# Kernel optimization log

Hardware: AMD Instinct MI355X
Metric: run time of the kernel (lower is better)

## Reference

```python
import jax, jax.numpy as jnp
import numpy as np

B, T, E, D = 64, 128, 4, 128
K = 4 * D  # ffn_hidden_dim
AUX_COEF = 0.01


def setup_inputs() -> dict:
    key = jax.random.key(0)
    ks = jax.random.split(key, 7)
    return {
        "x": jax.random.normal(ks[0], (B, T, D), dtype=jnp.float32),
        "expert_w1": jax.random.normal(ks[1], (T, E, D, K), dtype=jnp.float32) * 0.02,
        "expert_b1": jnp.zeros((T, E, K), dtype=jnp.float32),
        "expert_w2": jax.random.normal(ks[2], (T, E, K, D), dtype=jnp.float32) * 0.02,
        "expert_b2": jnp.zeros((T, E, D), dtype=jnp.float32),
        # router_train nn.Linear(D, E): store as [D, E] plus bias [E]
        "router_w": jax.random.normal(ks[3], (D, E), dtype=jnp.float32) * (1.0 / np.sqrt(D)),
        "router_b": jax.random.normal(ks[4], (E,), dtype=jnp.float32) * 0.01,
    }


def reference(x, expert_w1, expert_b1, expert_w2, expert_b2, router_w, router_b):
    # training=True path with use_relu_routing=True
    router_logits = jnp.einsum("btd,de->bte", x, router_w) + router_b  # [B,T,E]
    gates = jax.nn.relu(router_logits)
    gates = gates / (gates.sum(axis=-1, keepdims=True) + 1e-9)

    # per-token, per-expert 2-layer FFN
    hidden = jnp.einsum("btd,tedk->btek", x, expert_w1) + expert_b1  # [B,T,E,K]
    hidden = jax.nn.gelu(hidden, approximate=False)  # torch F.gelu default = exact erf
    expert_outputs = jnp.einsum("btek,tekd->bted", hidden, expert_w2) + expert_b2  # [B,T,E,D]

    output = (expert_outputs * gates[..., None]).sum(axis=2)  # [B,T,D]
    aux_loss = AUX_COEF * gates.sum() / (x.shape[0] * x.shape[1])
    return output, aux_loss
```

## Files before the change

### kernel.cpp

```cpp
#include <hip/hip_runtime.h>
#include <hip/hip_bf16.h>

#define NB 64
#define NT 128
#define NE 4
#define ND 128
#define NK 512

typedef __attribute__((ext_vector_type(8))) short bf16x8;
typedef __attribute__((ext_vector_type(4))) float f32x4;

__device__ __forceinline__ short f2bf(float f) {
    union { __hip_bfloat16 b; short s; } u;
    u.b = __float2bfloat16(f);
    return u.s;
}

__device__ __forceinline__ bf16x8 cvt8(const float* f) {
    bf16x8 r;
    #pragma unroll
    for (int j = 0; j < 8; ++j) r[j] = f2bf(f[j]);
    return r;
}

__device__ __forceinline__ float gelu_erf(float x) {
    return 0.5f * x * (1.0f + erff(x * 0.70710678118654752f));
}

__global__ __launch_bounds__(256)
void moe_gates(const float* __restrict__ x,
               const float* __restrict__ rw,
               const float* __restrict__ rb,
               float* __restrict__ gates_ws,
               float* __restrict__ aux_partial)
{
    const int tid  = threadIdx.x;
    const int lane = tid & 63;
    const int wave = tid >> 6;
    __shared__ float waux[4];

    const float4 rw0 = *(const float4*)(rw + lane * 4);
    const float4 rw1 = *(const float4*)(rw + (64 + lane) * 4);
    const float4 rbv = *(const float4*)rb;

    float aux = 0.f;
    #pragma unroll
    for (int i = 0; i < 4; ++i) {
        const int tok = (blockIdx.x * 4 + wave) * 4 + i;
        const float x0 = x[tok * ND + lane];
        const float x1 = x[tok * ND + 64 + lane];
        float p0 = x0 * rw0.x + x1 * rw1.x;
        float p1 = x0 * rw0.y + x1 * rw1.y;
        float p2 = x0 * rw0.z + x1 * rw1.z;
        float p3 = x0 * rw0.w + x1 * rw1.w;
        #pragma unroll
        for (int off = 32; off > 0; off >>= 1) {
            p0 += __shfl_xor(p0, off);
            p1 += __shfl_xor(p1, off);
            p2 += __shfl_xor(p2, off);
            p3 += __shfl_xor(p3, off);
        }
        if (lane == 0) {
            p0 = fmaxf(p0 + rbv.x, 0.f);
            p1 = fmaxf(p1 + rbv.y, 0.f);
            p2 = fmaxf(p2 + rbv.z, 0.f);
            p3 = fmaxf(p3 + rbv.w, 0.f);
            const float s   = p0 + p1 + p2 + p3;
            const float inv = 1.f / (s + 1e-9f);
            float4 g; g.x = p0 * inv; g.y = p1 * inv; g.z = p2 * inv; g.w = p3 * inv;
            *(float4*)(gates_ws + tok * NE) = g;
            aux += s * inv;
        }
    }
    if (lane == 0) waux[wave] = aux;
    __syncthreads();
    if (tid == 0)
        aux_partial[blockIdx.x] = waux[0] + waux[1] + waux[2] + waux[3];
}

__global__ __launch_bounds__(256, 2)
void moe_main(const float* __restrict__ x,
              const float* __restrict__ w1,
              const float* __restrict__ b1,
              const float* __restrict__ w2,
              const float* __restrict__ b2,
              const float* __restrict__ gates_ws,
              float* __restrict__ ws)
{
    const int bid  = blockIdx.x;
    const int t    = bid >> 2;
    const int e    = bid & 3;
    const int tid  = threadIdx.x;
    const int lane = tid & 63;
    const int wave = tid >> 6;
    const int l15  = lane & 15;
    const int l4   = lane >> 4;

    __shared__ short Hs[NB][NK + 8];
    __shared__ float gate_s[NB];

    if (tid < NB)
        gate_s[tid] = gates_ws[(tid * NT + t) * NE + e];

    const float* W1 = w1 + (size_t)((t * NE + e) * ND) * NK;
    const float* B1 = b1 + (t * NE + e) * NK;
    const int n0 = wave * 128;

    f32x4 acc[4][8];
    #pragma unroll
    for (int m = 0; m < 4; ++m)
        #pragma unroll
        for (int n = 0; n < 8; ++n) acc[m][n] = (f32x4){0.f, 0.f, 0.f, 0.f};

    {
        const float* wbase = W1 + (size_t)(l4 * 8) * NK + n0 + l15;
        float wbuf[4][8];
        #pragma unroll
        for (int q = 0; q < 4; ++q) {
            const float* wp = wbase + q * 16;
            #pragma unroll
            for (int j = 0; j < 8; ++j) wbuf[q][j] = wp[(size_t)j * NK];
        }

        bf16x8 afr[4];
        #pragma unroll
        for (int p = 0; p < 32; ++p) {
            const int ks = p >> 3, nt = p & 7;
            if (nt == 0) {
                const int d0 = ks * 32 + l4 * 8;
                #pragma unroll
                for (int m = 0; m < 4; ++m) {
                    const float* xp = x + (size_t)((m * 16 + l15) * NT + t) * ND + d0;
                    float xf[8];
                    *(float4*)&xf[0] = *(const float4*)(xp);
                    *(float4*)&xf[4] = *(const float4*)(xp + 4);
                    afr[m] = cvt8(xf);
                }
            }
            const bf16x8 bfr = cvt8(wbuf[p & 3]);
            if (p < 28) {
                const int p4 = p + 4;
                const int ks4 = p4 >> 3, nt4 = p4 & 7;
                const float* wp = wbase + (size_t)(ks4 * 32) * NK + nt4 * 16;
                #pragma unroll
                for (int j = 0; j < 8; ++j) wbuf[p4 & 3][j] = wp[(size_t)j * NK];
            }
            #pragma unroll
            for (int m = 0; m < 4; ++m)
                acc[m][nt] = __builtin_amdgcn_mfma_f32_16x16x32_bf16(afr[m], bfr, acc[m][nt], 0, 0, 0);
        }
    }

    #pragma unroll
    for (int nt = 0; nt < 8; ++nt) {
        const int n = n0 + nt * 16 + l15;
        const float bb = B1[n];
        #pragma unroll
        for (int m = 0; m < 4; ++m) {
            const int row = m * 16 + l4 * 4;
            #pragma unroll
            for (int r = 0; r < 4; ++r) {
                const float hh = acc[m][nt][r] + bb;
                Hs[row + r][n] = f2bf(gelu_erf(hh));
            }
        }
    }
    __syncthreads();

    const float* W2 = w2 + (size_t)((t * NE + e) * NK) * ND;
    const float* B2 = b2 + (t * NE + e) * ND;
    const int c0 = wave * 32;

    f32x4 acc2[4][2];
    #pragma unroll
    for (int m = 0; m < 4; ++m)
        #pragma unroll
        for (int n = 0; n < 2; ++n) acc2[m][n] = (f32x4){0.f, 0.f, 0.f, 0.f};

    {
        const float* w2base = W2 + (size_t)(l4 * 8) * ND + c0 + l15;
        float wb2[4][8];
        #pragma unroll
        for (int q = 0; q < 4; ++q) {
            const int ksq = q >> 1, ntq = q & 1;
            const float* wp = w2base + (size_t)(ksq * 32) * ND + ntq * 16;
            #pragma unroll
            for (int j = 0; j < 8; ++j) wb2[q][j] = wp[(size_t)j * ND];
        }

        bf16x8 a2[4];
        #pragma unroll
        for (int p = 0; p < 32; ++p) {
            const int ks = p >> 1, nt = p & 1;
            if (nt == 0) {
                const int k0 = ks * 32 + l4 * 8;
                #pragma unroll
                for (int m = 0; m < 4; ++m)
                    a2[m] = *(const bf16x8*)(&Hs[m * 16 + l15][k0]);
            }
            const bf16x8 bfr = cvt8(wb2[p & 3]);
            if (p < 28) {
                const int p4 = p + 4;
                const int ks4 = p4 >> 1, nt4 = p4 & 1;
                const float* wp = w2base + (size_t)(ks4 * 32) * ND + nt4 * 16;
                #pragma unroll
                for (int j = 0; j < 8; ++j) wb2[p4 & 3][j] = wp[(size_t)j * ND];
            }
            #pragma unroll
            for (int m = 0; m < 4; ++m)
                acc2[m][nt] = __builtin_amdgcn_mfma_f32_16x16x32_bf16(a2[m], bfr, acc2[m][nt], 0, 0, 0);
        }
    }

    #pragma unroll
    for (int nt = 0; nt < 2; ++nt) {
        const int c = c0 + nt * 16 + l15;
        const float bb = B2[c];
        #pragma unroll
        for (int m = 0; m < 4; ++m) {
            #pragma unroll
            for (int r = 0; r < 4; ++r) {
                const int b = m * 16 + l4 * 4 + r;
                const float v = (acc2[m][nt][r] + bb) * gate_s[b];
                ws[(size_t)(e * NB * NT + b * NT + t) * ND + c] = v;
            }
        }
    }
}

__global__ __launch_bounds__(256)
void moe_reduce(const float* __restrict__ ws,
                const float* __restrict__ aux_partial,
                float* __restrict__ out)
{
    const int i = blockIdx.x * blockDim.x + threadIdx.x;
    const int stride = NB * NT * ND / 4;
    const float4* w = (const float4*)ws;
    const float4 a = w[i];
    const float4 b = w[i + stride];
    const float4 c = w[i + 2 * stride];
    const float4 d = w[i + 3 * stride];
    float4 r;
    r.x = a.x + b.x + c.x + d.x;
    r.y = a.y + b.y + c.y + d.y;
    r.z = a.z + b.z + c.z + d.z;
    r.w = a.w + b.w + c.w + d.w;
    ((float4*)out)[i] = r;

    if (blockIdx.x == 0) {
        const int tid = threadIdx.x;
        float s = aux_partial[tid] + aux_partial[tid + 256];
        #pragma unroll
        for (int off = 32; off > 0; off >>= 1) s += __shfl_xor(s, off);
        __shared__ float wsum[4];
        if ((tid & 63) == 0) wsum[tid >> 6] = s;
        __syncthreads();
        if (tid == 0)
            out[NB * NT * ND] = (wsum[0] + wsum[1] + wsum[2] + wsum[3]) *
                                (0.01f / (NB * NT));
    }
}

__global__ __launch_bounds__(256, 2)
void moe_main_fb(const float* __restrict__ x,
                 const float* __restrict__ w1,
                 const float* __restrict__ b1,
                 const float* __restrict__ w2,
                 const float* __restrict__ b2,
                 const float* __restrict__ rw,
                 const float* __restrict__ rb,
                 float* __restrict__ out)
{
    const int blk  = blockIdx.x;
    const int t    = blk >> 2;
    const int e    = blk & 3;
    const int tid  = threadIdx.x;
    const int lane = tid & 63;
    const int wave = tid >> 6;
    const int l15  = lane & 15;
    const int l4   = lane >> 4;

    __shared__ short Hs[NB][NK + 8];
    __shared__ float gate_s[NB];

    if (tid < NB) {
        const int b = tid;
        const float* xr = x + (b * NT + t) * ND;
        float l0 = rb[0], l1 = rb[1], l2 = rb[2], l3 = rb[3];
        #pragma unroll 8
        for (int d = 0; d < ND; ++d) {
            const float xv = xr[d];
            const float* w = rw + d * NE;
            l0 += xv * w[0]; l1 += xv * w[1]; l2 += xv * w[2]; l3 += xv * w[3];
        }
        l0 = fmaxf(l0, 0.f); l1 = fmaxf(l1, 0.f); l2 = fmaxf(l2, 0.f); l3 = fmaxf(l3, 0.f);
        const float ss  = l0 + l1 + l2 + l3;
        const float inv = 1.f / (ss + 1e-9f);
        const float ge  = (e == 0) ? l0 : (e == 1) ? l1 : (e == 2) ? l2 : l3;
        gate_s[b] = ge * inv;
        if (e == 0) {
            float aux = ss * inv;
            #pragma unroll
            for (int off = 32; off > 0; off >>= 1) aux += __shfl_down(aux, off);
            if (lane == 0) atomicAdd(out + NB * NT * ND, aux * (0.01f / (NB * NT)));
        }
    }
    __syncthreads();

    const float* W1 = w1 + (size_t)((t * NE + e) * ND) * NK;
    const float* B1 = b1 + (t * NE + e) * NK;
    const int n0 = wave * 128;

    f32x4 acc[4][8];
    #pragma unroll
    for (int m = 0; m < 4; ++m)
        #pragma unroll
        for (int n = 0; n < 8; ++n) acc[m][n] = (f32x4){0.f, 0.f, 0.f, 0.f};

    #pragma unroll
    for (int ks = 0; ks < 4; ++ks) {
        const int d0 = ks * 32 + l4 * 8;
        bf16x8 afr[4];
        #pragma unroll
        for (int m = 0; m < 4; ++m) {
            const int b = m * 16 + l15;
            const float* xp = x + (b * NT + t) * ND + d0;
            float xf[8];
            *(float4*)&xf[0] = *(const float4*)(xp);
            *(float4*)&xf[4] = *(const float4*)(xp + 4);
            afr[m] = cvt8(xf);
        }
        #pragma unroll
        for (int nt = 0; nt < 8; ++nt) {
            const int n = n0 + nt * 16 + l15;
            const float* wp = W1 + (size_t)d0 * NK + n;
            float wf[8];
            #pragma unroll
            for (int j = 0; j < 8; ++j) wf[j] = wp[(size_t)j * NK];
            const bf16x8 bfr = cvt8(wf);
            #pragma unroll
            for (int m = 0; m < 4; ++m)
                acc[m][nt] = __builtin_amdgcn_mfma_f32_16x16x32_bf16(afr[m], bfr, acc[m][nt], 0, 0, 0);
        }
    }

    #pragma unroll
    for (int nt = 0; nt < 8; ++nt) {
        const int n = n0 + nt * 16 + l15;
        const float bb = B1[n];
        #pragma unroll
        for (int m = 0; m < 4; ++m) {
            const int row = m * 16 + l4 * 4;
            #pragma unroll
            for (int r = 0; r < 4; ++r) {
                const float hh = acc[m][nt][r] + bb;
                Hs[row + r][n] = f2bf(gelu_erf(hh));
            }
        }
    }
    __syncthreads();

    const float* W2 = w2 + (size_t)((t * NE + e) * NK) * ND;
    const float* B2 = b2 + (t * NE + e) * ND;
    const int c0 = wave * 32;

    f32x4 acc2[4][2];
    #pragma unroll
    for (int m = 0; m < 4; ++m)
        #pragma unroll
        for (int n = 0; n < 2; ++n) acc2[m][n] = (f32x4){0.f, 0.f, 0.f, 0.f};

    #pragma unroll 4
    for (int ks = 0; ks < 16; ++ks) {
        const int k0 = ks * 32 + l4 * 8;
        bf16x8 afr[4];
        #pragma unroll
        for (int m = 0; m < 4; ++m)
            afr[m] = *(const bf16x8*)(&Hs[m * 16 + l15][k0]);
        #pragma unroll
        for (int nt = 0; nt < 2; ++nt) {
            const int c = c0 + nt * 16 + l15;
            const float* wp = W2 + (size_t)k0 * ND + c;
            float wf[8];
            #pragma unroll
            for (int j = 0; j < 8; ++j) wf[j] = wp[(size_t)j * ND];
            const bf16x8 bfr = cvt8(wf);
            #pragma unroll
            for (int m = 0; m < 4; ++m)
                acc2[m][nt] = __builtin_amdgcn_mfma_f32_16x16x32_bf16(afr[m], bfr, acc2[m][nt], 0, 0, 0);
        }
    }

    #pragma unroll
    for (int nt = 0; nt < 2; ++nt) {
        const int c = c0 + nt * 16 + l15;
        const float bb = B2[c];
        #pragma unroll
        for (int m = 0; m < 4; ++m) {
            #pragma unroll
            for (int r = 0; r < 4; ++r) {
                const int b = m * 16 + l4 * 4 + r;
                const float v = (acc2[m][nt][r] + bb) * gate_s[b];
                atomicAdd(out + (size_t)(b * NT + t) * ND + c, v);
            }
        }
    }
}

extern "C" void kernel_launch(void* const* d_in, const int* in_sizes, int n_in,
                              void* d_out, int out_size, void* d_ws, size_t ws_size,
                              hipStream_t stream) {
    const float* x  = (const float*)d_in[0];
    const float* w1 = (const float*)d_in[1];
    const float* b1 = (const float*)d_in[2];
    const float* w2 = (const float*)d_in[3];
    const float* b2 = (const float*)d_in[4];
    const float* rw = (const float*)d_in[5];
    const float* rb = (const float*)d_in[6];
    float* out = (float*)d_out;

    const size_t contrib_elems = (size_t)NE * NB * NT * ND;
    const size_t gates_elems   = (size_t)NB * NT * NE;
    const size_t aux_elems     = 512;
    const size_t ws_need = (contrib_elems + gates_elems + aux_elems) * sizeof(float);

    if (ws_size >= ws_need) {
        float* contrib = (float*)d_ws;
        float* gates   = contrib + contrib_elems;
        float* auxp    = gates + gates_elems;

        moe_gates<<<512, 256, 0, stream>>>(x, rw, rb, gates, auxp);
        moe_main<<<NT * NE, 256, 0, stream>>>(x, w1, b1, w2, b2, gates, contrib);
        moe_reduce<<<(NB * NT * ND / 4) / 256, 256, 0, stream>>>(contrib, auxp, out);
    } else {
        hipMemsetAsync(d_out, 0, (size_t)(NB * NT * ND + 1) * sizeof(float), stream);
        moe_main_fb<<<NT * NE, 256, 0, stream>>>(x, w1, b1, w2, b2, rw, rb, out);
    }
}
```

Before: 70.71 us.

## Stage expert weights through LDS with coalesced float4 loads and double buffering

Weights used to be loaded straight from global memory with a column-strided scalar gather per lane. They are now read with coalesced float4 loads, converted to bf16 and staged in shared memory. W1 is double-buffered across 4 k-stages, and W2 is prefetched several stages ahead in registers before being written to an LDS buffer. This is meant to improve global memory coalescing and bandwidth. In exchange it uses about 75KB of LDS (W1 buffers aliased with the H buffer), which may limit occupancy to one block per CU. It also adds extra barriers, and reading B fragments as strided 2-byte LDS loads may cause bank conflicts.

```diff
diff --git a/kernel.cpp b/kernel.cpp
--- a/kernel.cpp
+++ b/kernel.cpp
@@ -8,6 +8,7 @@
 #define NK 512
 
 typedef __attribute__((ext_vector_type(8))) short bf16x8;
+typedef __attribute__((ext_vector_type(4))) short bf16x4;
 typedef __attribute__((ext_vector_type(4))) float f32x4;
 
 __device__ __forceinline__ short f2bf(float f) {
@@ -20,6 +21,12 @@
     bf16x8 r;
     #pragma unroll
     for (int j = 0; j < 8; ++j) r[j] = f2bf(f[j]);
+    return r;
+}
+
+__device__ __forceinline__ bf16x4 cvt4(float4 f) {
+    bf16x4 r;
+    r[0] = f2bf(f.x); r[1] = f2bf(f.y); r[2] = f2bf(f.z); r[3] = f2bf(f.w);
     return r;
 }
 
@@ -96,15 +103,21 @@
     const int l15  = lane & 15;
     const int l4   = lane >> 4;
 
-    __shared__ short Hs[NB][NK + 8];
-    __shared__ float gate_s[NB];
+    __shared__ __align__(16) char smem[75008];
+    short* W1s    = (short*)smem;
+    short* Hs     = (short*)smem;
+    short* W2s    = (short*)(smem + 66560);
+    float* gate_s = (float*)(smem + 74752);
 
     if (tid < NB)
         gate_s[tid] = gates_ws[(tid * NT + t) * NE + e];
 
     const float* W1 = w1 + (size_t)((t * NE + e) * ND) * NK;
     const float* B1 = b1 + (t * NE + e) * NK;
+    const float* W2 = w2 + (size_t)((t * NE + e) * NK) * ND;
+    const float* B2 = b2 + (t * NE + e) * ND;
     const int n0 = wave * 128;
+    const int c0 = wave * 32;
 
     f32x4 acc[4][8];
     #pragma unroll
@@ -113,42 +126,78 @@
         for (int n = 0; n < 8; ++n) acc[m][n] = (f32x4){0.f, 0.f, 0.f, 0.f};
 
     {
-        const float* wbase = W1 + (size_t)(l4 * 8) * NK + n0 + l15;
-        float wbuf[4][8];
-        #pragma unroll
-        for (int q = 0; q < 4; ++q) {
-            const float* wp = wbase + q * 16;
-            #pragma unroll
-            for (int j = 0; j < 8; ++j) wbuf[q][j] = wp[(size_t)j * NK];
-        }
-
+        float4 wv[16];
+        #pragma unroll
+        for (int q = 0; q < 16; ++q) {
+            const int f = q * 256 + tid;
+            wv[q] = *(const float4*)(W1 + (size_t)(f >> 7) * NK + (f & 127) * 4);
+        }
+        #pragma unroll
+        for (int q = 0; q < 16; ++q) {
+            const int f = q * 256 + tid;
+            *(bf16x4*)&W1s[(f >> 7) * 512 + (f & 127) * 4] = cvt4(wv[q]);
+        }
+        __syncthreads();
+    }
+
+    #pragma unroll
+    for (int s = 0; s < 4; ++s) {
+        const int cur = s & 1;
+        float4 wv[16];
+        if (s < 3) {
+            #pragma unroll
+            for (int q = 0; q < 16; ++q) {
+                const int f = q * 256 + tid;
+                wv[q] = *(const float4*)(W1 + (size_t)((s + 1) * 32 + (f >> 7)) * NK + (f & 127) * 4);
+            }
+        }
         bf16x8 afr[4];
         #pragma unroll
-        for (int p = 0; p < 32; ++p) {
-            const int ks = p >> 3, nt = p & 7;
-            if (nt == 0) {
-                const int d0 = ks * 32 + l4 * 8;
-                #pragma unroll
-                for (int m = 0; m < 4; ++m) {
-                    const float* xp = x + (size_t)((m * 16 + l15) * NT + t) * ND + d0;
-                    float xf[8];
-                    *(float4*)&xf[0] = *(const float4*)(xp);
-                    *(float4*)&xf[4] = *(const float4*)(xp + 4);
-                    afr[m] = cvt8(xf);
-                }
-            }
-            const bf16x8 bfr = cvt8(wbuf[p & 3]);
-            if (p < 28) {
-                const int p4 = p + 4;
-                const int ks4 = p4 >> 3, nt4 = p4 & 7;
-                const float* wp = wbase + (size_t)(ks4 * 32) * NK + nt4 * 16;
-                #pragma unroll
-                for (int j = 0; j < 8; ++j) wbuf[p4 & 3][j] = wp[(size_t)j * NK];
-            }
+        for (int m = 0; m < 4; ++m) {
+            const float* xp = x + (size_t)((m * 16 + l15) * NT + t) * ND + s * 32 + l4 * 8;
+            float xf[8];
+            *(float4*)&xf[0] = *(const float4*)(xp);
+            *(float4*)&xf[4] = *(const float4*)(xp + 4);
+            afr[m] = cvt8(xf);
+        }
+        #pragma unroll
+        for (int nt = 0; nt < 8; ++nt) {
+            const int n = n0 + nt * 16 + l15;
+            bf16x8 bfr;
+            #pragma unroll
+            for (int j = 0; j < 8; ++j)
+                bfr[j] = W1s[cur * 16384 + (l4 * 8 + j) * 512 + n];
             #pragma unroll
             for (int m = 0; m < 4; ++m)
                 acc[m][nt] = __builtin_amdgcn_mfma_f32_16x16x32_bf16(afr[m], bfr, acc[m][nt], 0, 0, 0);
         }
+        if (s < 3) {
+            const int nxt = cur ^ 1;
+            #pragma unroll
+            for (int q = 0; q < 16; ++q) {
+                const int f = q * 256 + tid;
+                *(bf16x4*)&W1s[nxt * 16384 + (f >> 7) * 512 + (f & 127) * 4] = cvt4(wv[q]);
+            }
+        }
+        __syncthreads();
+    }
+
+    float4 w20[4];
+    float4 nv[3][4];
+    #pragma unroll
+    for (int q = 0; q < 4; ++q) {
+        const int f = q * 256 + tid;
+        w20[q] = *(const float4*)(W2 + (size_t)(f >> 5) * ND + (f & 31) * 4);
+    }
+    #pragma unroll
+    for (int q = 0; q < 4; ++q) {
+        const int f = q * 256 + tid;
+        nv[0][q] = *(const float4*)(W2 + (size_t)(32 + (f >> 5)) * ND + (f & 31) * 4);
+    }
+    #pragma unroll
+    for (int q = 0; q < 4; ++q) {
+        const int f = q * 256 + tid;
+        nv[1][q] = *(const float4*)(W2 + (size_t)(64 + (f >> 5)) * ND + (f & 31) * 4);
     }
 
     #pragma unroll
@@ -161,54 +210,56 @@
             #pragma unroll
             for (int r = 0; r < 4; ++r) {
                 const float hh = acc[m][nt][r] + bb;
-                Hs[row + r][n] = f2bf(gelu_erf(hh));
-            }
-        }
+                Hs[(row + r) * 520 + n] = f2bf(gelu_erf(hh));
+            }
+        }
+    }
+    #pragma unroll
+    for (int q = 0; q < 4; ++q) {
+        const int f = q * 256 + tid;
+        *(bf16x4*)&W2s[(f >> 5) * 128 + (f & 31) * 4] = cvt4(w20[q]);
     }
     __syncthreads();
 
-    const float* W2 = w2 + (size_t)((t * NE + e) * NK) * ND;
-    const float* B2 = b2 + (t * NE + e) * ND;
-    const int c0 = wave * 32;
-
     f32x4 acc2[4][2];
     #pragma unroll
     for (int m = 0; m < 4; ++m)
         #pragma unroll
         for (int n = 0; n < 2; ++n) acc2[m][n] = (f32x4){0.f, 0.f, 0.f, 0.f};
 
-    {
-        const float* w2base = W2 + (size_t)(l4 * 8) * ND + c0 + l15;
-        float wb2[4][8];
-        #pragma unroll
-        for (int q = 0; q < 4; ++q) {
-            const int ksq = q >> 1, ntq = q & 1;
-            const float* wp = w2base + (size_t)(ksq * 32) * ND + ntq * 16;
-            #pragma unroll
-            for (int j = 0; j < 8; ++j) wb2[q][j] = wp[(size_t)j * ND];
-        }
-
+    #pragma unroll
+    for (int s = 0; s < 16; ++s) {
+        if (s + 3 <= 15) {
+            #pragma unroll
+            for (int q = 0; q < 4; ++q) {
+                const int f = q * 256 + tid;
+                nv[(s + 2) % 3][q] =
+                    *(const float4*)(W2 + (size_t)((s + 3) * 32 + (f >> 5)) * ND + (f & 31) * 4);
+            }
+        }
         bf16x8 a2[4];
         #pragma unroll
-        for (int p = 0; p < 32; ++p) {
-            const int ks = p >> 1, nt = p & 1;
-            if (nt == 0) {
-                const int k0 = ks * 32 + l4 * 8;
-                #pragma unroll
-                for (int m = 0; m < 4; ++m)
-                    a2[m] = *(const bf16x8*)(&Hs[m * 16 + l15][k0]);
-            }
-            const bf16x8 bfr = cvt8(wb2[p & 3]);
-            if (p < 28) {
-                const int p4 = p + 4;
-                const int ks4 = p4 >> 1, nt4 = p4 & 1;
-                const float* wp = w2base + (size_t)(ks4 * 32) * ND + nt4 * 16;
-                #pragma unroll
-                for (int j = 0; j < 8; ++j) wb2[p4 & 3][j] = wp[(size_t)j * ND];
-            }
+        for (int m = 0; m < 4; ++m)
+            a2[m] = *(const bf16x8*)&Hs[(m * 16 + l15) * 520 + s * 32 + l4 * 8];
+        #pragma unroll
+        for (int nt = 0; nt < 2; ++nt) {
+            const int c = c0 + nt * 16 + l15;
+            bf16x8 bfr;
+            #pragma unroll
+            for (int j = 0; j < 8; ++j)
+                bfr[j] = W2s[(l4 * 8 + j) * 128 + c];
             #pragma unroll
             for (int m = 0; m < 4; ++m)
                 acc2[m][nt] = __builtin_amdgcn_mfma_f32_16x16x32_bf16(a2[m], bfr, acc2[m][nt], 0, 0, 0);
+        }
+        if (s < 15) {
+            __syncthreads();
+            #pragma unroll
+            for (int q = 0; q < 4; ++q) {
+                const int f = q * 256 + tid;
+                *(bf16x4*)&W2s[(f >> 5) * 128 + (f & 31) * 4] = cvt4(nv[s % 3][q]);
+            }
+            __syncthreads();
         }
     }
 
```

After: 71.83 us. Within noise of the previous version (+1.6%).

## Split batch rows across four blocks per token-expert pair

Applied to the files above, without the earlier changes.

Each (token, expert) block is split into four blocks that each process 16 batch rows instead of 64. The activation fragments are loaded once up front, accumulators and shared memory shrink, and launch bounds are raised to allow more resident blocks. This aims for more parallelism and occupancy, but each expert's weights are now streamed by four blocks, so global weight traffic can quadruple unless the cache absorbs the repeats.

```diff
diff --git a/kernel.cpp b/kernel.cpp
--- a/kernel.cpp
+++ b/kernel.cpp
@@ -6,6 +6,7 @@
 #define NE 4
 #define ND 128
 #define NK 512
+#define MH 16
 
 typedef __attribute__((ext_vector_type(8))) short bf16x8;
 typedef __attribute__((ext_vector_type(4))) float f32x4;
@@ -78,7 +79,7 @@
         aux_partial[blockIdx.x] = waux[0] + waux[1] + waux[2] + waux[3];
 }
 
-__global__ __launch_bounds__(256, 2)
+__global__ __launch_bounds__(256, 5)
 void moe_main(const float* __restrict__ x,
               const float* __restrict__ w1,
               const float* __restrict__ b1,
@@ -88,29 +89,42 @@
               float* __restrict__ ws)
 {
     const int bid  = blockIdx.x;
-    const int t    = bid >> 2;
-    const int e    = bid & 3;
+    const int h    = bid & 3;
+    const int s    = bid >> 2;
+    const int t    = s >> 2;
+    const int e    = s & 3;
     const int tid  = threadIdx.x;
     const int lane = tid & 63;
     const int wave = tid >> 6;
     const int l15  = lane & 15;
     const int l4   = lane >> 4;
 
-    __shared__ short Hs[NB][NK + 8];
-    __shared__ float gate_s[NB];
-
-    if (tid < NB)
-        gate_s[tid] = gates_ws[(tid * NT + t) * NE + e];
+    __shared__ short Hs[MH][NK + 8];
+    __shared__ float gate_s[MH];
+
+    if (tid < MH)
+        gate_s[tid] = gates_ws[((h * MH + tid) * NT + t) * NE + e];
 
     const float* W1 = w1 + (size_t)((t * NE + e) * ND) * NK;
     const float* B1 = b1 + (t * NE + e) * NK;
     const int n0 = wave * 128;
 
-    f32x4 acc[4][8];
-    #pragma unroll
-    for (int m = 0; m < 4; ++m)
-        #pragma unroll
-        for (int n = 0; n < 8; ++n) acc[m][n] = (f32x4){0.f, 0.f, 0.f, 0.f};
+    bf16x8 afr[4];
+    {
+        float xa[4][8];
+        #pragma unroll
+        for (int ks = 0; ks < 4; ++ks) {
+            const float* xp = x + (size_t)((h * MH + l15) * NT + t) * ND + ks * 32 + l4 * 8;
+            *(float4*)&xa[ks][0] = *(const float4*)(xp);
+            *(float4*)&xa[ks][4] = *(const float4*)(xp + 4);
+        }
+        #pragma unroll
+        for (int ks = 0; ks < 4; ++ks) afr[ks] = cvt8(xa[ks]);
+    }
+
+    f32x4 acc[8];
+    #pragma unroll
+    for (int n = 0; n < 8; ++n) acc[n] = (f32x4){0.f, 0.f, 0.f, 0.f};
 
     {
         const float* wbase = W1 + (size_t)(l4 * 8) * NK + n0 + l15;
@@ -122,21 +136,9 @@
             for (int j = 0; j < 8; ++j) wbuf[q][j] = wp[(size_t)j * NK];
         }
 
-        bf16x8 afr[4];
         #pragma unroll
         for (int p = 0; p < 32; ++p) {
             const int ks = p >> 3, nt = p & 7;
-            if (nt == 0) {
-                const int d0 = ks * 32 + l4 * 8;
-                #pragma unroll
-                for (int m = 0; m < 4; ++m) {
-                    const float* xp = x + (size_t)((m * 16 + l15) * NT + t) * ND + d0;
-                    float xf[8];
-                    *(float4*)&xf[0] = *(const float4*)(xp);
-                    *(float4*)&xf[4] = *(const float4*)(xp + 4);
-                    afr[m] = cvt8(xf);
-                }
-            }
             const bf16x8 bfr = cvt8(wbuf[p & 3]);
             if (p < 28) {
                 const int p4 = p + 4;
@@ -145,9 +147,7 @@
                 #pragma unroll
                 for (int j = 0; j < 8; ++j) wbuf[p4 & 3][j] = wp[(size_t)j * NK];
             }
-            #pragma unroll
-            for (int m = 0; m < 4; ++m)
-                acc[m][nt] = __builtin_amdgcn_mfma_f32_16x16x32_bf16(afr[m], bfr, acc[m][nt], 0, 0, 0);
+            acc[nt] = __builtin_amdgcn_mfma_f32_16x16x32_bf16(afr[ks], bfr, acc[nt], 0, 0, 0);
         }
     }
 
@@ -156,13 +156,9 @@
         const int n = n0 + nt * 16 + l15;
         const float bb = B1[n];
         #pragma unroll
-        for (int m = 0; m < 4; ++m) {
-            const int row = m * 16 + l4 * 4;
-            #pragma unroll
-            for (int r = 0; r < 4; ++r) {
-                const float hh = acc[m][nt][r] + bb;
-                Hs[row + r][n] = f2bf(gelu_erf(hh));
-            }
+        for (int r = 0; r < 4; ++r) {
+            const float hh = acc[nt][r] + bb;
+            Hs[l4 * 4 + r][n] = f2bf(gelu_erf(hh));
         }
     }
     __syncthreads();
@@ -171,11 +167,9 @@
     const float* B2 = b2 + (t * NE + e) * ND;
     const int c0 = wave * 32;
 
-    f32x4 acc2[4][2];
-    #pragma unroll
-    for (int m = 0; m < 4; ++m)
-        #pragma unroll
-        for (int n = 0; n < 2; ++n) acc2[m][n] = (f32x4){0.f, 0.f, 0.f, 0.f};
+    f32x4 acc2[2];
+    #pragma unroll
+    for (int n = 0; n < 2; ++n) acc2[n] = (f32x4){0.f, 0.f, 0.f, 0.f};
 
     {
         const float* w2base = W2 + (size_t)(l4 * 8) * ND + c0 + l15;
@@ -188,16 +182,12 @@
             for (int j = 0; j < 8; ++j) wb2[q][j] = wp[(size_t)j * ND];
         }
 
-        bf16x8 a2[4];
+        bf16x8 a2;
         #pragma unroll
         for (int p = 0; p < 32; ++p) {
             const int ks = p >> 1, nt = p & 1;
-            if (nt == 0) {
-                const int k0 = ks * 32 + l4 * 8;
-                #pragma unroll
-                for (int m = 0; m < 4; ++m)
-                    a2[m] = *(const bf16x8*)(&Hs[m * 16 + l15][k0]);
-            }
+            if (nt == 0)
+                a2 = *(const bf16x8*)&Hs[l15][ks * 32 + l4 * 8];
             const bf16x8 bfr = cvt8(wb2[p & 3]);
             if (p < 28) {
                 const int p4 = p + 4;
@@ -206,9 +196,7 @@
                 #pragma unroll
                 for (int j = 0; j < 8; ++j) wb2[p4 & 3][j] = wp[(size_t)j * ND];
             }
-            #pragma unroll
-            for (int m = 0; m < 4; ++m)
-                acc2[m][nt] = __builtin_amdgcn_mfma_f32_16x16x32_bf16(a2[m], bfr, acc2[m][nt], 0, 0, 0);
+            acc2[nt] = __builtin_amdgcn_mfma_f32_16x16x32_bf16(a2, bfr, acc2[nt], 0, 0, 0);
         }
     }
 
@@ -217,13 +205,11 @@
         const int c = c0 + nt * 16 + l15;
         const float bb = B2[c];
         #pragma unroll
-        for (int m = 0; m < 4; ++m) {
-            #pragma unroll
-            for (int r = 0; r < 4; ++r) {
-                const int b = m * 16 + l4 * 4 + r;
-                const float v = (acc2[m][nt][r] + bb) * gate_s[b];
-                ws[(size_t)(e * NB * NT + b * NT + t) * ND + c] = v;
-            }
+        for (int r = 0; r < 4; ++r) {
+            const int bl = l4 * 4 + r;
+            const int b  = h * MH + bl;
+            const float v = (acc2[nt][r] + bb) * gate_s[bl];
+            ws[(size_t)(e * NB * NT + b * NT + t) * ND + c] = v;
         }
     }
 }
@@ -430,7 +416,7 @@
         float* auxp    = gates + gates_elems;
 
         moe_gates<<<512, 256, 0, stream>>>(x, rw, rb, gates, auxp);
-        moe_main<<<NT * NE, 256, 0, stream>>>(x, w1, b1, w2, b2, gates, contrib);
+        moe_main<<<NT * NE * 4, 256, 0, stream>>>(x, w1, b1, w2, b2, gates, contrib);
         moe_reduce<<<(NB * NT * ND / 4) / 256, 256, 0, stream>>>(contrib, auxp, out);
     } else {
         hipMemsetAsync(d_out, 0, (size_t)(NB * NT * ND + 1) * sizeof(float), stream);
```

Measured after the change: 170.5 us. 2.41x slower.
